# Kernel tuning notes

Hardware: AMD Instinct MI355X
Metric: run time of the kernel (lower is better)

Reference implementation:

```python
import jax, jax.numpy as jnp
import numpy as np

D = 512          # hidden_dim
H_HEADS = 8
DH = D // H_HEADS  # 64
L = 6            # n_layers
P = 8            # patch size
KT = 3           # temporal kernel
Z_DIM = 32
FILM_SCALE = 0.5
ROPE_BASE = 10000.0
EPS = 1e-5


def layer_norm(x, g, b):
    mu = x.mean(-1, keepdims=True)
    var = ((x - mu) ** 2).mean(-1, keepdims=True)
    return (x - mu) * jax.lax.rsqrt(var + EPS) * g + b


def rotate_half(x):
    x1, x2 = jnp.split(x, 2, axis=-1)
    return jnp.concatenate([-x2, x1], axis=-1)


def rope_time(T, dtype):
    half = DH // 2
    inv_freq = ROPE_BASE ** (-(jnp.arange(half, dtype=dtype) / half))  # (half,)
    angles = jnp.arange(T, dtype=dtype)[:, None] * inv_freq[None, :]   # (T, half)
    sin = jnp.concatenate([jnp.sin(angles), jnp.sin(angles)], -1)      # (T, DH)
    cos = jnp.concatenate([jnp.cos(angles), jnp.cos(angles)], -1)
    return sin, cos


def setup_inputs() -> dict:
    key = jax.random.key(0)
    ks = iter(jax.random.split(key, 64))
    n = lambda shape, s=0.02: jax.random.normal(next(ks), shape, jnp.float32) * s
    inp = {
        "x": jax.random.normal(next(ks), (16, 32, 3, 64, 64), jnp.float32),
        "z": jax.random.normal(next(ks), (16, 32, Z_DIM), jnp.float32),
        # tokenizer: CausalConv3d (kt,ph,pw)=(3,8,8), stride (1,8,8)
        "conv_w": n((D, 3, KT, P, P)),
        "conv_b": jnp.zeros((D,), jnp.float32),
        "tok_g": jnp.ones((D,), jnp.float32),
        "tok_b": jnp.zeros((D,), jnp.float32),
        # FiLM from z -> (gamma, beta)
        "film_w": n((Z_DIM, 2 * D)),
        "film_b": jnp.zeros((2 * D,), jnp.float32),
        # transformer blocks (stacked over L)
        "ln1_g": jnp.ones((L, D), jnp.float32), "ln1_b": jnp.zeros((L, D), jnp.float32),
        "kqv_w": n((L, D, 3 * D)), "kqv_b": jnp.zeros((L, 3 * D), jnp.float32),
        "proj_w": n((L, D, D)), "proj_b": jnp.zeros((L, D), jnp.float32),
        "ln2_g": jnp.ones((L, D), jnp.float32), "ln2_b": jnp.zeros((L, D), jnp.float32),
        "mlp_w1": n((L, D, 4 * D)), "mlp_b1": jnp.zeros((L, 4 * D), jnp.float32),
        "mlp_w2": n((L, 4 * D, D)), "mlp_b2": jnp.zeros((L, D), jnp.float32),
        "rs_attn": jnp.full((L,), 0.5, jnp.float32),
        "rs_mlp": jnp.full((L,), 0.5, jnp.float32),
        # scoring head
        "head_g": jnp.ones((D,), jnp.float32), "head_b": jnp.zeros((D,), jnp.float32),
        "head_w": n((D, 1)), "head_bias": jnp.zeros((1,), jnp.float32),
    }
    return inp


def _forward(x, z, conv_w, conv_b, tok_g, tok_b, film_w, film_b,
             ln1_g, ln1_b, kqv_w, kqv_b, proj_w, proj_b, ln2_g, ln2_b,
             mlp_w1, mlp_b1, mlp_w2, mlp_b2, rs_attn, rs_mlp,
             head_g, head_b, head_w, head_bias):
    B, T, C, Himg, Wimg = x.shape
    # ---- SpatialTemporalTokenizer: causal Conv3d (pad time on past only) ----
    xc = jnp.transpose(x, (0, 2, 1, 3, 4))  # [B,C,T,H,W]
    y = jax.lax.conv_general_dilated(
        xc, conv_w, window_strides=(1, P, P),
        padding=[(KT - 1, 0), (0, 0), (0, 0)],
        dimension_numbers=("NCDHW", "OIDHW", "NCDHW"))
    y = y + conv_b[None, :, None, None, None]          # [B,D,T,Hn,Wn]
    Hn, Wn = y.shape[3], y.shape[4]
    tok = jnp.transpose(y, (0, 2, 3, 4, 1)).reshape(B, T, Hn * Wn, D)
    tok = layer_norm(tok, tok_g, tok_b)                 # [B,T,N,D]
    # ---- FiLM conditioning from z ----
    gb = z @ film_w + film_b                            # [B,T,2D]
    gamma, beta = jnp.split(gb, 2, axis=-1)
    tok = (1.0 + FILM_SCALE * gamma)[:, :, None, :] * tok + (FILM_SCALE * beta)[:, :, None, :]
    # ---- spatial pooling -> temporal sequence ----
    h = tok.mean(axis=2)                                # [B,T,D]
    # ---- transformer stack (causal, time RoPE, pre-LN, gated residuals) ----
    sin_t, cos_t = rope_time(T, h.dtype)                # (T, DH)
    causal = jnp.tril(jnp.ones((T, T), bool))
    neg_inf = jnp.finfo(h.dtype).min
    for i in range(L):
        xi = layer_norm(h, ln1_g[i], ln1_b[i])
        kqv = xi @ kqv_w[i] + kqv_b[i]                  # [B,T,3D]
        k, q, v = jnp.split(kqv, 3, axis=-1)            # torch chunk order: k,q,v
        sh = lambda t: t.reshape(B, T, H_HEADS, DH).transpose(0, 2, 1, 3)  # [B,h,T,d]
        q, k, v = sh(q), sh(k), sh(v)
        q = q * cos_t + rotate_half(q) * sin_t
        k = k * cos_t + rotate_half(k) * sin_t
        att = jnp.einsum("bhqd,bhkd->bhqk", q, k) / np.sqrt(DH)
        att = jnp.where(causal[None, None], att, neg_inf)
        att = jax.nn.softmax(att, axis=-1)
        yv = jnp.einsum("bhqk,bhkd->bhqd", att, v)
        yv = yv.transpose(0, 2, 1, 3).reshape(B, T, D)
        attn_out = yv @ proj_w[i] + proj_b[i]
        h = h + rs_attn[i] * attn_out
        x2 = layer_norm(h, ln2_g[i], ln2_b[i])
        m = jax.nn.gelu(x2 @ mlp_w1[i] + mlp_b1[i], approximate=False) @ mlp_w2[i] + mlp_b2[i]
        h = h + rs_mlp[i] * m
    # ---- per-timestep score head ----
    h = layer_norm(h, head_g, head_b)
    score = (h @ head_w + head_bias)[..., 0]            # [B,T]
    return score


def reference(x, z, conv_w, conv_b, tok_g, tok_b, film_w, film_b,
              ln1_g, ln1_b, kqv_w, kqv_b, proj_w, proj_b, ln2_g, ln2_b,
              mlp_w1, mlp_b1, mlp_w2, mlp_b2, rs_attn, rs_mlp,
              head_g, head_b, head_w, head_bias):
    return _forward(x, z, conv_w, conv_b, tok_g, tok_b, film_w, film_b,
                    ln1_g, ln1_b, kqv_w, kqv_b, proj_w, proj_b, ln2_g, ln2_b,
                    mlp_w1, mlp_b1, mlp_w2, mlp_b2, rs_attn, rs_mlp,
                    head_g, head_b, head_w, head_bias)
```

## Files before the change

### kernel.cpp

```cpp
#include <hip/hip_runtime.h>
#include <math.h>

#define EPS 1e-5f

typedef __attribute__((ext_vector_type(8))) short short8;
typedef __attribute__((ext_vector_type(4))) float f32x4;

__device__ __forceinline__ short f2bf(float f) {
    unsigned u = __float_as_uint(f);
    u += 0x7fffu + ((u >> 16) & 1u);
    return (short)(u >> 16);
}
__device__ __forceinline__ float bf2f(short s) {
    return __uint_as_float(((unsigned)(unsigned short)s) << 16);
}
__device__ __forceinline__ void async16(const void* g, void* l) {
    __builtin_amdgcn_global_load_lds(
        (const __attribute__((address_space(1))) unsigned*)g,
        (__attribute__((address_space(3))) unsigned*)l, 16, 0, 0);
}

__device__ __forceinline__ float block_reduce_sum_256(float v, float* red) {
    #pragma unroll
    for (int o = 32; o > 0; o >>= 1) v += __shfl_down(v, o, 64);
    __syncthreads();
    if ((threadIdx.x & 63) == 0) red[threadIdx.x >> 6] = v;
    __syncthreads();
    return red[0] + red[1] + red[2] + red[3];
}

__global__ __launch_bounds__(256) void prep_misc(
    const float* __restrict__ z, const float* __restrict__ fw,
    const float* __restrict__ fb, float* __restrict__ gb,
    const float* __restrict__ conv_w, short* __restrict__ wbf,
    const float* __restrict__ x, short* __restrict__ xbf) {
    __shared__ float zs[32];
    int bi = blockIdx.x, tid = threadIdx.x;
    if (bi < 512) {
        if (tid < 32) zs[tid] = z[bi * 32 + tid];
        __syncthreads();
        for (int j = tid; j < 1024; j += 256) {
            float acc = fb[j];
            #pragma unroll
            for (int k = 0; k < 32; k++) acc = fmaf(zs[k], fw[k * 1024 + j], acc);
            gb[bi * 1024 + j] = acc;
        }
    } else if (bi < 1664) {
        int i = (bi - 512) * 256 + tid;
        wbf[i] = f2bf(conv_w[i]);
    } else {
        int i = (bi - 1664) * 256 + tid;
        float4 a = *(const float4*)(x + (size_t)i * 8);
        float4 b = *(const float4*)(x + (size_t)i * 8 + 4);
        short8 o = {f2bf(a.x), f2bf(a.y), f2bf(a.z), f2bf(a.w),
                    f2bf(b.x), f2bf(b.y), f2bf(b.z), f2bf(b.w)};
        *(short8*)(xbf + (size_t)i * 8) = o;
    }
}

__global__ __launch_bounds__(256) void prep_tcast(
    const float* __restrict__ kqv_w, short* __restrict__ kqvT,
    const float* __restrict__ proj_w, short* __restrict__ projT,
    const float* __restrict__ mlp_w1, short* __restrict__ mlp1T,
    const float* __restrict__ mlp_w2, short* __restrict__ mlp2T) {
    __shared__ float tile[32][33];
    int bi = blockIdx.x;
    const float* src; short* dst; int NT, K, N, rel;
    if (bi < 4608)       { src = kqv_w;  dst = kqvT;  NT = 48; K = 512;  N = 1536; rel = bi; }
    else if (bi < 6144)  { src = proj_w; dst = projT; NT = 16; K = 512;  N = 512;  rel = bi - 4608; }
    else if (bi < 12288) { src = mlp_w1; dst = mlp1T; NT = 64; K = 512;  N = 2048; rel = bi - 6144; }
    else                 { src = mlp_w2; dst = mlp2T; NT = 16; K = 2048; N = 512;  rel = bi - 12288; }
    int per = NT * (K / 32);
    int layer = rel / per, r2 = rel - layer * per;
    int nt = r2 % NT, kt = r2 / NT;
    src += (size_t)layer * K * N;
    dst += (size_t)layer * N * K;
    int n0 = nt * 32, k0 = kt * 32;
    int lx = threadIdx.x & 31, ly = threadIdx.x >> 5;
    #pragma unroll
    for (int i = 0; i < 32; i += 8)
        tile[ly + i][lx] = src[(size_t)(k0 + ly + i) * N + n0 + lx];
    __syncthreads();
    #pragma unroll
    for (int i = 0; i < 32; i += 8)
        dst[(size_t)(n0 + ly + i) * K + k0 + lx] = f2bf(tile[lx][ly + i]);
}

__global__ __launch_bounds__(256) void conv_gemm(
    const short* __restrict__ xbf, const short* __restrict__ wbf,
    const float* __restrict__ cb, short* __restrict__ tok) {
    __shared__ short As[128 * 64];
    __shared__ short Bs[128 * 64];
    int tid = threadIdx.x;
    int n0 = blockIdx.x * 128, m0 = blockIdx.y * 128;
    int wave = tid >> 6, lane = tid & 63, quad = lane >> 4, l16 = lane & 15;
    int wm = wave & 1, wn = wave >> 1;

    int segA[4], tA[4];
    long long base0[4];
    #pragma unroll
    for (int e = 0; e < 4; e++) {
        int p = e * 256 + tid;
        int row = p >> 3;
        segA[e] = (p & 7) ^ (row & 7);
        int m = m0 + row;
        int bt = m >> 6, nn = m & 63;
        int b = bt >> 5, t = bt & 31;
        int hn = nn >> 3, wn2 = nn & 7;
        tA[e] = t;
        base0[e] = (((long long)(b * 32 + t - 2) * 3) << 12)
                   + (long long)(hn * 8) * 64 + wn2 * 8;
    }

    f32x4 acc[4][4];
    #pragma unroll
    for (int mt = 0; mt < 4; mt++)
        #pragma unroll
        for (int nt = 0; nt < 4; nt++) acc[mt][nt] = (f32x4){0.f, 0.f, 0.f, 0.f};

    for (int k0 = 0; k0 < 576; k0 += 64) {
        #pragma unroll
        for (int e = 0; e < 4; e++) {
            int p = e * 256 + tid;
            int n = p >> 3, seg = (p & 7) ^ (n & 7);
            async16(wbf + (size_t)(n0 + n) * 576 + k0 + seg * 8, Bs + p * 8);
        }
        #pragma unroll
        for (int e = 0; e < 4; e++) {
            int p = e * 256 + tid;
            int ks = (k0 >> 3) + segA[e];
            int ch = (ks >= 24) + (ks >= 48);
            int r = ks - ch * 24;
            int kt = r >> 3, ph = r & 7;
            short8 v8 = (short8){0, 0, 0, 0, 0, 0, 0, 0};
            if (tA[e] + kt >= 2)
                v8 = *(const short8*)(xbf + base0[e]
                        + ((long long)(kt * 3 + ch) << 12) + ph * 64);
            *(short8*)(As + p * 8) = v8;
        }
        __syncthreads();
        #pragma unroll
        for (int ksub = 0; ksub < 2; ksub++) {
            int ccb = ksub * 4 + quad;
            short8 af[4], bf[4];
            #pragma unroll
            for (int mt = 0; mt < 4; mt++) {
                int row = wm * 64 + mt * 16 + l16;
                af[mt] = *(const short8*)(As + (row * 8 + (ccb ^ (row & 7))) * 8);
            }
            #pragma unroll
            for (int nt = 0; nt < 4; nt++) {
                int row = wn * 64 + nt * 16 + l16;
                bf[nt] = *(const short8*)(Bs + (row * 8 + (ccb ^ (row & 7))) * 8);
            }
            #pragma unroll
            for (int mt = 0; mt < 4; mt++)
                #pragma unroll
                for (int nt = 0; nt < 4; nt++)
                    acc[mt][nt] = __builtin_amdgcn_mfma_f32_16x16x32_bf16(
                        af[mt], bf[nt], acc[mt][nt], 0, 0, 0);
        }
        __syncthreads();
    }
    #pragma unroll
    for (int mt = 0; mt < 4; mt++)
        #pragma unroll
        for (int nt = 0; nt < 4; nt++)
            #pragma unroll
            for (int reg = 0; reg < 4; reg++) {
                int m = m0 + wm * 64 + mt * 16 + quad * 4 + reg;
                int n = n0 + wn * 64 + nt * 16 + l16;
                tok[(size_t)m * 512 + n] = f2bf(acc[mt][nt][reg] + cb[n]);
            }
}

__global__ __launch_bounds__(256) void tok_post(
    const short* __restrict__ tok, const float* __restrict__ tg,
    const float* __restrict__ tb, const float* __restrict__ gb,
    float* __restrict__ h) {
    __shared__ float mu_s[64], inv_s[64];
    __shared__ float red[4][512];
    int bt = blockIdx.x, tid = threadIdx.x;
    int wave = tid >> 6, lane = tid & 63;
    {
        int tokn = wave * 16 + (lane >> 2), part = lane & 3;
        const short* p = tok + (size_t)(bt * 64 + tokn) * 512 + part * 128;
        float s = 0.f, ss = 0.f;
        #pragma unroll
        for (int i = 0; i < 16; i++) {
            short8 v = *(const short8*)(p + i * 8);
            #pragma unroll
            for (int j = 0; j < 8; j++) {
                float f = bf2f(v[j]);
                s += f; ss += f * f;
            }
        }
        s += __shfl_xor(s, 1, 64); ss += __shfl_xor(ss, 1, 64);
        s += __shfl_xor(s, 2, 64); ss += __shfl_xor(ss, 2, 64);
        if (part == 0) {
            float mu = s * (1.f / 512.f);
            float var = ss * (1.f / 512.f) - mu * mu;
            mu_s[tokn] = mu;
            inv_s[tokn] = rsqrtf(var + EPS);
        }
    }
    __syncthreads();
    float hacc[8] = {0.f, 0.f, 0.f, 0.f, 0.f, 0.f, 0.f, 0.f};
    int c0 = lane * 8;
    for (int it = 0; it < 16; it++) {
        int n = it * 4 + wave;
        float mu = mu_s[n], inv = inv_s[n];
        short8 v = *(const short8*)(tok + (size_t)(bt * 64 + n) * 512 + c0);
        #pragma unroll
        for (int j = 0; j < 8; j++) hacc[j] += (bf2f(v[j]) - mu) * inv;
    }
    #pragma unroll
    for (int j = 0; j < 8; j++) red[wave][c0 + j] = hacc[j];
    __syncthreads();
    #pragma unroll
    for (int cc = 0; cc < 2; cc++) {
        int c = tid + cc * 256;
        float S = red[0][c] + red[1][c] + red[2][c] + red[3][c];
        float G  = 1.f + 0.5f * gb[bt * 1024 + c];
        float Be = 0.5f * gb[bt * 1024 + 512 + c];
        h[bt * 512 + c] = G * (tg[c] * (S * (1.f / 64.f)) + tb[c]) + Be;
    }
}

__global__ __launch_bounds__(256) void attn_fused(
    const float* __restrict__ hsrc, const float* __restrict__ lng,
    const float* __restrict__ lnb, const short* __restrict__ Bw,
    const float* __restrict__ bias, short* __restrict__ yv) {
    __shared__ char smem[57344] __attribute__((aligned(16)));
    __shared__ float mu_s[32], inv_s[32];
    short* As = (short*)smem;
    short* Bs = (short*)(smem + 32768);
    float (*qs)[64] = (float(*)[64])(smem);
    float (*ks)[64] = (float(*)[64])(smem + 8192);
    float (*vs)[64] = (float(*)[64])(smem + 16384);
    float (*qr)[64] = (float(*)[64])(smem + 24576);
    float (*kr)[64] = (float(*)[64])(smem + 32768);
    float (*att)[32] = (float(*)[32])(smem + 40960);
    int blk = blockIdx.x, b = blk >> 3, hh = blk & 7;
    int tid = threadIdx.x;
    int m0 = b * 32;
    {
        int row = tid >> 3, l8 = tid & 7;
        const float* hp = hsrc + (size_t)(m0 + row) * 512 + l8 * 64;
        float s = 0.f, ss = 0.f;
        #pragma unroll
        for (int i = 0; i < 16; i++) {
            float4 v = *(const float4*)(hp + i * 4);
            s += v.x + v.y + v.z + v.w;
            ss += v.x * v.x + v.y * v.y + v.z * v.z + v.w * v.w;
        }
        s += __shfl_xor(s, 1, 64); ss += __shfl_xor(ss, 1, 64);
        s += __shfl_xor(s, 2, 64); ss += __shfl_xor(ss, 2, 64);
        s += __shfl_xor(s, 4, 64); ss += __shfl_xor(ss, 4, 64);
        if (l8 == 0) {
            float mu = s * (1.f / 512.f);
            float var = ss * (1.f / 512.f) - mu * mu;
            mu_s[row] = mu;
            inv_s[row] = rsqrtf(var + EPS);
        }
    }
    __syncthreads();
    #pragma unroll
    for (int e = 0; e < 8; e++) {
        int lc = e * 256 + tid;
        int row = lc >> 6, cc = lc & 63;
        float mu = mu_s[row], inv = inv_s[row];
        const float* hp = hsrc + (size_t)(m0 + row) * 512 + cc * 8;
        float4 a = *(const float4*)hp, b2 = *(const float4*)(hp + 4);
        float4 g0 = *(const float4*)(lng + cc * 8), g1 = *(const float4*)(lng + cc * 8 + 4);
        float4 b0 = *(const float4*)(lnb + cc * 8), b1 = *(const float4*)(lnb + cc * 8 + 4);
        short8 o = {f2bf((a.x - mu) * inv * g0.x + b0.x),
                    f2bf((a.y - mu) * inv * g0.y + b0.y),
                    f2bf((a.z - mu) * inv * g0.z + b0.z),
                    f2bf((a.w - mu) * inv * g0.w + b0.w),
                    f2bf((b2.x - mu) * inv * g1.x + b1.x),
                    f2bf((b2.y - mu) * inv * g1.y + b1.y),
                    f2bf((b2.z - mu) * inv * g1.z + b1.z),
                    f2bf((b2.w - mu) * inv * g1.w + b1.w)};
        *(short8*)(As + (row * 64 + (cc ^ (row & 7))) * 8) = o;
    }
    __syncthreads();
    int wave = tid >> 6, lane = tid & 63, quad = lane >> 4, l16 = lane & 15;
    f32x4 acc[2][3];
    #pragma unroll
    for (int m2 = 0; m2 < 2; m2++)
        #pragma unroll
        for (int g = 0; g < 3; g++) acc[m2][g] = (f32x4){0.f, 0.f, 0.f, 0.f};
    for (int k0 = 0; k0 < 512; k0 += 64) {
        #pragma unroll
        for (int e = 0; e < 6; e++) {
            int p = e * 256 + tid;
            int row = p >> 3, seg = (p & 7) ^ (row & 7);
            int n = ((row >> 6) << 9) + hh * 64 + (row & 63);
            async16(Bw + (size_t)n * 512 + k0 + seg * 8, Bs + p * 8);
        }
        __syncthreads();
        #pragma unroll
        for (int ksub = 0; ksub < 2; ksub++) {
            int ccb = ksub * 4 + quad;
            short8 af[2], bf[3];
            #pragma unroll
            for (int m2 = 0; m2 < 2; m2++) {
                int row = m2 * 16 + l16;
                int cc = (k0 >> 3) + ccb;
                af[m2] = *(const short8*)(As + (row * 64 + (cc ^ (row & 7))) * 8);
            }
            #pragma unroll
            for (int g = 0; g < 3; g++) {
                int row = g * 64 + wave * 16 + l16;
                bf[g] = *(const short8*)(Bs + (row * 8 + (ccb ^ (row & 7))) * 8);
            }
            #pragma unroll
            for (int m2 = 0; m2 < 2; m2++)
                #pragma unroll
                for (int g = 0; g < 3; g++)
                    acc[m2][g] = __builtin_amdgcn_mfma_f32_16x16x32_bf16(
                        af[m2], bf[g], acc[m2][g], 0, 0, 0);
        }
        __syncthreads();
    }
    float bb0 = bias[hh * 64 + wave * 16 + l16];
    float bb1 = bias[512 + hh * 64 + wave * 16 + l16];
    float bb2 = bias[1024 + hh * 64 + wave * 16 + l16];
    int dcol = wave * 16 + l16;
    #pragma unroll
    for (int m2 = 0; m2 < 2; m2++)
        #pragma unroll
        for (int reg = 0; reg < 4; reg++) {
            int tkn = m2 * 16 + quad * 4 + reg;
            ks[tkn][dcol] = acc[m2][0][reg] + bb0;
            qs[tkn][dcol] = acc[m2][1][reg] + bb1;
            vs[tkn][dcol] = acc[m2][2][reg] + bb2;
        }
    __syncthreads();
    const float lnb_c = logf(10000.f) / 32.f;
    for (int idx = tid; idx < 2048; idx += 256) {
        int t = idx >> 6, d = idx & 63;
        int j = d & 31;
        float ang = (float)t * expf(-(float)j * lnb_c);
        float sv = sinf(ang), cv = cosf(ang);
        float qv = qs[t][d], kv = ks[t][d];
        float qo = qs[t][d ^ 32], ko = ks[t][d ^ 32];
        float rq = (d < 32) ? -qo : qo;
        float rk = (d < 32) ? -ko : ko;
        qr[t][d] = qv * cv + rq * sv;
        kr[t][d] = kv * cv + rk * sv;
    }
    __syncthreads();
    #pragma unroll
    for (int l = 0; l < 4; l++) {
        int idx = l * 256 + tid;
        int qt = idx >> 5, kt2 = idx & 31;
        float s;
        if (kt2 > qt) {
            s = -1e30f;
        } else {
            float a = 0.f;
            #pragma unroll
            for (int d = 0; d < 64; d++) a = fmaf(qr[qt][d], kr[kt2][d], a);
            s = a * 0.125f;
        }
        att[qt][kt2] = s;
    }
    __syncthreads();
    if (tid < 32) {
        float m = -1e30f;
        #pragma unroll
        for (int k = 0; k < 32; k++) m = fmaxf(m, att[tid][k]);
        float sum = 0.f;
        #pragma unroll
        for (int k = 0; k < 32; k++) {
            float e = expf(att[tid][k] - m);
            att[tid][k] = e;
            sum += e;
        }
        float inv = 1.f / sum;
        #pragma unroll
        for (int k = 0; k < 32; k++) att[tid][k] *= inv;
    }
    __syncthreads();
    for (int idx = tid; idx < 2048; idx += 256) {
        int t = idx >> 6, d = idx & 63;
        float a = 0.f;
        #pragma unroll
        for (int k = 0; k < 32; k++) a = fmaf(att[t][k], vs[k][d], a);
        yv[(size_t)(b * 32 + t) * 512 + hh * 64 + d] = f2bf(a);
    }
}

__global__ __launch_bounds__(256) void gemm_ln(
    const float* __restrict__ hsrc, const float* __restrict__ lng,
    const float* __restrict__ lnb, const short* __restrict__ Bw,
    const float* __restrict__ bias, int N, int mode,
    float* __restrict__ outf, short* __restrict__ outb) {
    __shared__ short As[32 * 512];
    __shared__ short Bs[128 * 128];
    __shared__ float mu_s[32], inv_s[32];
    int tid = threadIdx.x;
    int m0 = blockIdx.y * 32, n0 = blockIdx.x * 128;
    {
        int row = tid >> 3, l8 = tid & 7;
        const float* hp = hsrc + (size_t)(m0 + row) * 512 + l8 * 64;
        float s = 0.f, ss = 0.f;
        #pragma unroll
        for (int i = 0; i < 16; i++) {
            float4 v = *(const float4*)(hp + i * 4);
            s += v.x + v.y + v.z + v.w;
            ss += v.x * v.x + v.y * v.y + v.z * v.z + v.w * v.w;
        }
        s += __shfl_xor(s, 1, 64); ss += __shfl_xor(ss, 1, 64);
        s += __shfl_xor(s, 2, 64); ss += __shfl_xor(ss, 2, 64);
        s += __shfl_xor(s, 4, 64); ss += __shfl_xor(ss, 4, 64);
        if (l8 == 0) {
            float mu = s * (1.f / 512.f);
            float var = ss * (1.f / 512.f) - mu * mu;
            mu_s[row] = mu;
            inv_s[row] = rsqrtf(var + EPS);
        }
    }
    __syncthreads();
    #pragma unroll
    for (int e = 0; e < 8; e++) {
        int lc = e * 256 + tid;
        int row = lc >> 6, cc = lc & 63;
        float mu = mu_s[row], inv = inv_s[row];
        const float* hp = hsrc + (size_t)(m0 + row) * 512 + cc * 8;
        float4 a = *(const float4*)hp, b = *(const float4*)(hp + 4);
        float4 g0 = *(const float4*)(lng + cc * 8), g1 = *(const float4*)(lng + cc * 8 + 4);
        float4 b0 = *(const float4*)(lnb + cc * 8), b1 = *(const float4*)(lnb + cc * 8 + 4);
        short8 o = {f2bf((a.x - mu) * inv * g0.x + b0.x),
                    f2bf((a.y - mu) * inv * g0.y + b0.y),
                    f2bf((a.z - mu) * inv * g0.z + b0.z),
                    f2bf((a.w - mu) * inv * g0.w + b0.w),
                    f2bf((b.x - mu) * inv * g1.x + b1.x),
                    f2bf((b.y - mu) * inv * g1.y + b1.y),
                    f2bf((b.z - mu) * inv * g1.z + b1.z),
                    f2bf((b.w - mu) * inv * g1.w + b1.w)};
        *(short8*)(As + (row * 64 + (cc ^ (row & 7))) * 8) = o;
    }
    __syncthreads();
    int wave = tid >> 6, lane = tid & 63, quad = lane >> 4, l16 = lane & 15;
    f32x4 acc[2][2];
    #pragma unroll
    for (int a2 = 0; a2 < 2; a2++)
        #pragma unroll
        for (int b2 = 0; b2 < 2; b2++) acc[a2][b2] = (f32x4){0.f, 0.f, 0.f, 0.f};
    for (int k0 = 0; k0 < 512; k0 += 128) {
        #pragma unroll
        for (int e = 0; e < 8; e++) {
            int p = e * 256 + tid;
            int row = p >> 4, seg = (p & 15) ^ (row & 15);
            async16(Bw + (size_t)(n0 + row) * 512 + k0 + seg * 8, Bs + p * 8);
        }
        __syncthreads();
        #pragma unroll
        for (int ksub = 0; ksub < 4; ksub++) {
            int ccb = ksub * 4 + quad;
            short8 af[2], bf[2];
            #pragma unroll
            for (int m2 = 0; m2 < 2; m2++) {
                int row = m2 * 16 + l16;
                int cc = (k0 >> 3) + ccb;
                af[m2] = *(const short8*)(As + (row * 64 + (cc ^ (row & 7))) * 8);
            }
            #pragma unroll
            for (int n2 = 0; n2 < 2; n2++) {
                int row = wave * 32 + n2 * 16 + l16;
                bf[n2] = *(const short8*)(Bs + (row * 16 + (ccb ^ (row & 15))) * 8);
            }
            #pragma unroll
            for (int m2 = 0; m2 < 2; m2++)
                #pragma unroll
                for (int n2 = 0; n2 < 2; n2++)
                    acc[m2][n2] = __builtin_amdgcn_mfma_f32_16x16x32_bf16(
                        af[m2], bf[n2], acc[m2][n2], 0, 0, 0);
        }
        __syncthreads();
    }
    #pragma unroll
    for (int m2 = 0; m2 < 2; m2++)
        #pragma unroll
        for (int n2 = 0; n2 < 2; n2++)
            #pragma unroll
            for (int reg = 0; reg < 4; reg++) {
                int m = m0 + m2 * 16 + quad * 4 + reg;
                int n = n0 + wave * 32 + n2 * 16 + l16;
                float v = acc[m2][n2][reg] + bias[n];
                if (mode == 1) {
                    v = 0.5f * v * (1.f + erff(v * 0.70710678118f));
                    outb[(size_t)m * N + n] = f2bf(v);
                } else {
                    outf[(size_t)m * N + n] = v;
                }
            }
}

__global__ __launch_bounds__(256) void gemm_res(
    const short* __restrict__ Ag, const short* __restrict__ Bw,
    const float* __restrict__ bias, const float* __restrict__ rsPtr,
    float* __restrict__ hm, int K) {
    __shared__ short As[32 * 128];
    __shared__ short Bs[64 * 128];
    int tid = threadIdx.x;
    int m0 = blockIdx.y * 32, n0 = blockIdx.x * 64;
    int wave = tid >> 6, lane = tid & 63, quad = lane >> 4, l16 = lane & 15;
    f32x4 acc[2];
    acc[0] = (f32x4){0.f, 0.f, 0.f, 0.f};
    acc[1] = (f32x4){0.f, 0.f, 0.f, 0.f};
    for (int k0 = 0; k0 < K; k0 += 128) {
        #pragma unroll
        for (int e = 0; e < 2; e++) {
            int p = e * 256 + tid;
            int row = p >> 4, seg = (p & 15) ^ (row & 15);
            async16(Ag + (size_t)(m0 + row) * K + k0 + seg * 8, As + p * 8);
        }
        #pragma unroll
        for (int e = 0; e < 4; e++) {
            int p = e * 256 + tid;
            int row = p >> 4, seg = (p & 15) ^ (row & 15);
            async16(Bw + (size_t)(n0 + row) * K + k0 + seg * 8, Bs + p * 8);
        }
        __syncthreads();
        #pragma unroll
        for (int ksub = 0; ksub < 4; ksub++) {
            int ccb = ksub * 4 + quad;
            short8 bf;
            {
                int row = wave * 16 + l16;
                bf = *(const short8*)(Bs + (row * 16 + (ccb ^ (row & 15))) * 8);
            }
            #pragma unroll
            for (int m2 = 0; m2 < 2; m2++) {
                int row = m2 * 16 + l16;
                short8 af = *(const short8*)(As + (row * 16 + (ccb ^ (row & 15))) * 8);
                acc[m2] = __builtin_amdgcn_mfma_f32_16x16x32_bf16(af, bf, acc[m2], 0, 0, 0);
            }
        }
        __syncthreads();
    }
    float rsv = *rsPtr;
    #pragma unroll
    for (int m2 = 0; m2 < 2; m2++)
        #pragma unroll
        for (int reg = 0; reg < 4; reg++) {
            int m = m0 + m2 * 16 + quad * 4 + reg;
            int n = n0 + wave * 16 + l16;
            size_t off = (size_t)m * 512 + n;
            hm[off] = hm[off] + rsv * (acc[m2][reg] + bias[n]);
        }
}

__global__ __launch_bounds__(256) void head_kernel(
    const float* __restrict__ h, const float* __restrict__ g,
    const float* __restrict__ bb, const float* __restrict__ w,
    const float* __restrict__ bias0, float* __restrict__ out) {
    __shared__ float red[8];
    int token = blockIdx.x, tid = threadIdx.x;
    float v0 = h[token * 512 + tid], v1 = h[token * 512 + tid + 256];
    float s  = block_reduce_sum_256(v0 + v1, red);
    float ss = block_reduce_sum_256(v0 * v0 + v1 * v1, red);
    float mu = s * (1.f / 512.f);
    float var = ss * (1.f / 512.f) - mu * mu;
    float inv = rsqrtf(var + EPS);
    float n0 = (v0 - mu) * inv * g[tid] + bb[tid];
    float n1 = (v1 - mu) * inv * g[tid + 256] + bb[tid + 256];
    float dot = block_reduce_sum_256(n0 * w[tid] + n1 * w[tid + 256], red);
    if (tid == 0) out[token] = dot + bias0[0];
}

extern "C" void kernel_launch(void* const* d_in, const int* in_sizes, int n_in,
                              void* d_out, int out_size, void* d_ws, size_t ws_size,
                              hipStream_t stream) {
    const float* x       = (const float*)d_in[0];
    const float* z       = (const float*)d_in[1];
    const float* conv_w  = (const float*)d_in[2];
    const float* conv_b  = (const float*)d_in[3];
    const float* tok_g   = (const float*)d_in[4];
    const float* tok_b   = (const float*)d_in[5];
    const float* film_w  = (const float*)d_in[6];
    const float* film_b  = (const float*)d_in[7];
    const float* ln1_g   = (const float*)d_in[8];
    const float* ln1_b   = (const float*)d_in[9];
    const float* kqv_w   = (const float*)d_in[10];
    const float* kqv_b   = (const float*)d_in[11];
    const float* proj_w  = (const float*)d_in[12];
    const float* proj_b  = (const float*)d_in[13];
    const float* ln2_g   = (const float*)d_in[14];
    const float* ln2_b   = (const float*)d_in[15];
    const float* mlp_w1  = (const float*)d_in[16];
    const float* mlp_b1  = (const float*)d_in[17];
    const float* mlp_w2  = (const float*)d_in[18];
    const float* mlp_b2  = (const float*)d_in[19];
    const float* rs_attn = (const float*)d_in[20];
    const float* rs_mlp  = (const float*)d_in[21];
    const float* head_g  = (const float*)d_in[22];
    const float* head_b  = (const float*)d_in[23];
    const float* head_w  = (const float*)d_in[24];
    const float* head_bs = (const float*)d_in[25];
    float* out = (float*)d_out;

    float* ws = (float*)d_ws;
    float* gb   = ws;
    float* h    = gb + 524288;
    short* sb = (short*)(h + 262144);
    short* wbf   = sb;
    short* kqvT  = wbf   + 294912;
    short* projT = kqvT  + 4718592;
    short* mlp1T = projT + 1572864;
    short* mlp2T = mlp1T + 6291456;
    short* tokb  = mlp2T + 6291456;
    short* yvb   = tokb  + 16777216;
    short* mbuf  = yvb   + 262144;
    short* xbf   = mbuf  + 1048576;

    prep_misc<<<4736, 256, 0, stream>>>(z, film_w, film_b, gb, conv_w, wbf, x, xbf);
    prep_tcast<<<18432, 256, 0, stream>>>(kqv_w, kqvT, proj_w, projT,
                                          mlp_w1, mlp1T, mlp_w2, mlp2T);

    conv_gemm<<<dim3(4, 256), 256, 0, stream>>>(xbf, wbf, conv_b, tokb);
    tok_post<<<512, 256, 0, stream>>>(tokb, tok_g, tok_b, gb, h);

    for (int i = 0; i < 6; i++) {
        attn_fused<<<128, 256, 0, stream>>>(
            h, ln1_g + i * 512, ln1_b + i * 512,
            kqvT + (size_t)i * 1536 * 512, kqv_b + i * 1536, yvb);
        gemm_res<<<dim3(8, 16), 256, 0, stream>>>(
            yvb, projT + (size_t)i * 512 * 512, proj_b + i * 512,
            rs_attn + i, h, 512);
        gemm_ln<<<dim3(16, 16), 256, 0, stream>>>(
            h, ln2_g + i * 512, ln2_b + i * 512,
            mlp1T + (size_t)i * 2048 * 512, mlp_b1 + i * 2048,
            2048, 1, nullptr, mbuf);
        gemm_res<<<dim3(8, 16), 256, 0, stream>>>(
            mbuf, mlp2T + (size_t)i * 512 * 2048, mlp_b2 + i * 512,
            rs_mlp + i, h, 2048);
    }

    head_kernel<<<512, 256, 0, stream>>>(h, head_g, head_b, head_w, head_bs, out);
}
```

Measured before the change: 549.8 us.

## Fuse conv GEMM with token LayerNorm pooling, split-K residual GEMMs, vectorize transpose

Merges the tokenizer conv GEMM and the tok_post LayerNorm/mean-pool/FiLM pass into one kernel with one block per (b,t). The block computes all 512 output channels for its 64 patches and reduces them in registers, so the large bf16 token buffer is never written or read back. The residual GEMMs (proj and MLP2) now use split-K over blockIdx.z and accumulate into h with atomicAdd, which adds more blocks for small grids at the cost of atomics and non-deterministic summation order. The weight-transpose store also now writes short2 pairs.

```diff
diff --git a/kernel.cpp b/kernel.cpp
--- a/kernel.cpp
+++ b/kernel.cpp
@@ -81,150 +81,144 @@
     for (int i = 0; i < 32; i += 8)
         tile[ly + i][lx] = src[(size_t)(k0 + ly + i) * N + n0 + lx];
     __syncthreads();
-    #pragma unroll
-    for (int i = 0; i < 32; i += 8)
-        dst[(size_t)(n0 + ly + i) * K + k0 + lx] = f2bf(tile[lx][ly + i]);
-}
-
-__global__ __launch_bounds__(256) void conv_gemm(
+    int kp = threadIdx.x & 15, nn = threadIdx.x >> 4;
+    #pragma unroll
+    for (int i = 0; i < 2; i++) {
+        int row = nn + i * 16;
+        short2 o = {f2bf(tile[kp * 2][row]), f2bf(tile[kp * 2 + 1][row])};
+        *(short2*)(dst + (size_t)(n0 + row) * K + k0 + kp * 2) = o;
+    }
+}
+
+__global__ __launch_bounds__(256, 2) void conv_fused(
     const short* __restrict__ xbf, const short* __restrict__ wbf,
-    const float* __restrict__ cb, short* __restrict__ tok) {
-    __shared__ short As[128 * 64];
-    __shared__ short Bs[128 * 64];
+    const float* __restrict__ cb, const float* __restrict__ tg,
+    const float* __restrict__ tb, const float* __restrict__ gb,
+    float* __restrict__ h) {
+    __shared__ short As[64 * 32];
+    __shared__ short Bs[512 * 32];
+    __shared__ float redsum[4][64], redss[4][64];
+    __shared__ float mu_s[64], inv_s[64];
+    int bt = blockIdx.x, b = bt >> 5, t = bt & 31;
     int tid = threadIdx.x;
-    int n0 = blockIdx.x * 128, m0 = blockIdx.y * 128;
     int wave = tid >> 6, lane = tid & 63, quad = lane >> 4, l16 = lane & 15;
-    int wm = wave & 1, wn = wave >> 1;
-
-    int segA[4], tA[4];
-    long long base0[4];
-    #pragma unroll
-    for (int e = 0; e < 4; e++) {
-        int p = e * 256 + tid;
-        int row = p >> 3;
-        segA[e] = (p & 7) ^ (row & 7);
-        int m = m0 + row;
-        int bt = m >> 6, nn = m & 63;
-        int b = bt >> 5, t = bt & 31;
-        int hn = nn >> 3, wn2 = nn & 7;
-        tA[e] = t;
-        base0[e] = (((long long)(b * 32 + t - 2) * 3) << 12)
-                   + (long long)(hn * 8) * 64 + wn2 * 8;
-    }
-
-    f32x4 acc[4][4];
+
+    int rowA = tid >> 2;
+    int cA = (tid & 3) ^ ((rowA >> 1) & 3);
+    int hn = rowA >> 3, wn2 = rowA & 7;
+    long long baseA = (((long long)(b * 32 + t - 2) * 3) << 12)
+                      + (long long)(hn * 8) * 64 + wn2 * 8;
+
+    f32x4 acc[4][8];
     #pragma unroll
     for (int mt = 0; mt < 4; mt++)
         #pragma unroll
-        for (int nt = 0; nt < 4; nt++) acc[mt][nt] = (f32x4){0.f, 0.f, 0.f, 0.f};
-
-    for (int k0 = 0; k0 < 576; k0 += 64) {
-        #pragma unroll
-        for (int e = 0; e < 4; e++) {
-            int p = e * 256 + tid;
-            int n = p >> 3, seg = (p & 7) ^ (n & 7);
-            async16(wbf + (size_t)(n0 + n) * 576 + k0 + seg * 8, Bs + p * 8);
-        }
-        #pragma unroll
-        for (int e = 0; e < 4; e++) {
-            int p = e * 256 + tid;
-            int ks = (k0 >> 3) + segA[e];
+        for (int nt = 0; nt < 8; nt++) acc[mt][nt] = (f32x4){0.f, 0.f, 0.f, 0.f};
+
+    for (int k0 = 0; k0 < 576; k0 += 32) {
+        #pragma unroll
+        for (int e = 0; e < 8; e++) {
+            int s = e * 256 + tid;
+            int n = s >> 2;
+            int c = (s & 3) ^ ((n >> 1) & 3);
+            async16(wbf + (size_t)n * 576 + k0 + c * 8, Bs + s * 8);
+        }
+        {
+            int ks = (k0 >> 3) + cA;
             int ch = (ks >= 24) + (ks >= 48);
             int r = ks - ch * 24;
             int kt = r >> 3, ph = r & 7;
             short8 v8 = (short8){0, 0, 0, 0, 0, 0, 0, 0};
-            if (tA[e] + kt >= 2)
-                v8 = *(const short8*)(xbf + base0[e]
+            if (t + kt >= 2)
+                v8 = *(const short8*)(xbf + baseA
                         + ((long long)(kt * 3 + ch) << 12) + ph * 64);
-            *(short8*)(As + p * 8) = v8;
-        }
-        __syncthreads();
-        #pragma unroll
-        for (int ksub = 0; ksub < 2; ksub++) {
-            int ccb = ksub * 4 + quad;
-            short8 af[4], bf[4];
-            #pragma unroll
-            for (int mt = 0; mt < 4; mt++) {
-                int row = wm * 64 + mt * 16 + l16;
-                af[mt] = *(const short8*)(As + (row * 8 + (ccb ^ (row & 7))) * 8);
-            }
-            #pragma unroll
-            for (int nt = 0; nt < 4; nt++) {
-                int row = wn * 64 + nt * 16 + l16;
-                bf[nt] = *(const short8*)(Bs + (row * 8 + (ccb ^ (row & 7))) * 8);
-            }
-            #pragma unroll
-            for (int mt = 0; mt < 4; mt++)
-                #pragma unroll
-                for (int nt = 0; nt < 4; nt++)
-                    acc[mt][nt] = __builtin_amdgcn_mfma_f32_16x16x32_bf16(
-                        af[mt], bf[nt], acc[mt][nt], 0, 0, 0);
-        }
-        __syncthreads();
+            *(short8*)(As + tid * 8) = v8;
+        }
+        __syncthreads();
+        short8 af[4], bf[8];
+        #pragma unroll
+        for (int mt = 0; mt < 4; mt++) {
+            int row = mt * 16 + l16;
+            int pc = quad ^ ((row >> 1) & 3);
+            af[mt] = *(const short8*)(As + row * 32 + pc * 8);
+        }
+        #pragma unroll
+        for (int nt = 0; nt < 8; nt++) {
+            int row = wave * 128 + nt * 16 + l16;
+            int pc = quad ^ ((row >> 1) & 3);
+            bf[nt] = *(const short8*)(Bs + row * 32 + pc * 8);
+        }
+        #pragma unroll
+        for (int mt = 0; mt < 4; mt++)
+            #pragma unroll
+            for (int nt = 0; nt < 8; nt++)
+                acc[mt][nt] = __builtin_amdgcn_mfma_f32_16x16x32_bf16(
+                    af[mt], bf[nt], acc[mt][nt], 0, 0, 0);
+        __syncthreads();
+    }
+
+    float cbn[8], tgn[8], tbn[8], Gn[8], Ben[8];
+    #pragma unroll
+    for (int nt = 0; nt < 8; nt++) {
+        int n = wave * 128 + nt * 16 + l16;
+        cbn[nt] = cb[n]; tgn[nt] = tg[n]; tbn[nt] = tb[n];
+        Gn[nt]  = 1.f + 0.5f * gb[bt * 1024 + n];
+        Ben[nt] = 0.5f * gb[bt * 1024 + 512 + n];
     }
     #pragma unroll
     for (int mt = 0; mt < 4; mt++)
         #pragma unroll
-        for (int nt = 0; nt < 4; nt++)
-            #pragma unroll
-            for (int reg = 0; reg < 4; reg++) {
-                int m = m0 + wm * 64 + mt * 16 + quad * 4 + reg;
-                int n = n0 + wn * 64 + nt * 16 + l16;
-                tok[(size_t)m * 512 + n] = f2bf(acc[mt][nt][reg] + cb[n]);
-            }
-}
-
-__global__ __launch_bounds__(256) void tok_post(
-    const short* __restrict__ tok, const float* __restrict__ tg,
-    const float* __restrict__ tb, const float* __restrict__ gb,
-    float* __restrict__ h) {
-    __shared__ float mu_s[64], inv_s[64];
-    __shared__ float red[4][512];
-    int bt = blockIdx.x, tid = threadIdx.x;
-    int wave = tid >> 6, lane = tid & 63;
-    {
-        int tokn = wave * 16 + (lane >> 2), part = lane & 3;
-        const short* p = tok + (size_t)(bt * 64 + tokn) * 512 + part * 128;
-        float s = 0.f, ss = 0.f;
-        #pragma unroll
-        for (int i = 0; i < 16; i++) {
-            short8 v = *(const short8*)(p + i * 8);
-            #pragma unroll
-            for (int j = 0; j < 8; j++) {
-                float f = bf2f(v[j]);
-                s += f; ss += f * f;
-            }
-        }
-        s += __shfl_xor(s, 1, 64); ss += __shfl_xor(ss, 1, 64);
-        s += __shfl_xor(s, 2, 64); ss += __shfl_xor(ss, 2, 64);
-        if (part == 0) {
-            float mu = s * (1.f / 512.f);
-            float var = ss * (1.f / 512.f) - mu * mu;
-            mu_s[tokn] = mu;
-            inv_s[tokn] = rsqrtf(var + EPS);
-        }
+        for (int reg = 0; reg < 4; reg++) {
+            float s = 0.f, ss = 0.f;
+            #pragma unroll
+            for (int nt = 0; nt < 8; nt++) {
+                float v = acc[mt][nt][reg] + cbn[nt];
+                s += v; ss += v * v;
+            }
+            #pragma unroll
+            for (int o = 1; o < 16; o <<= 1) {
+                s  += __shfl_xor(s, o, 64);
+                ss += __shfl_xor(ss, o, 64);
+            }
+            if (l16 == 0) {
+                int m = mt * 16 + quad * 4 + reg;
+                redsum[wave][m] = s; redss[wave][m] = ss;
+            }
+        }
+    __syncthreads();
+    if (tid < 64) {
+        float S  = redsum[0][tid] + redsum[1][tid] + redsum[2][tid] + redsum[3][tid];
+        float SS = redss[0][tid] + redss[1][tid] + redss[2][tid] + redss[3][tid];
+        float mu = S * (1.f / 512.f);
+        float var = SS * (1.f / 512.f) - mu * mu;
+        mu_s[tid] = mu; inv_s[tid] = rsqrtf(var + EPS);
     }
     __syncthreads();
     float hacc[8] = {0.f, 0.f, 0.f, 0.f, 0.f, 0.f, 0.f, 0.f};
-    int c0 = lane * 8;
-    for (int it = 0; it < 16; it++) {
-        int n = it * 4 + wave;
-        float mu = mu_s[n], inv = inv_s[n];
-        short8 v = *(const short8*)(tok + (size_t)(bt * 64 + n) * 512 + c0);
-        #pragma unroll
-        for (int j = 0; j < 8; j++) hacc[j] += (bf2f(v[j]) - mu) * inv;
-    }
-    #pragma unroll
-    for (int j = 0; j < 8; j++) red[wave][c0 + j] = hacc[j];
-    __syncthreads();
-    #pragma unroll
-    for (int cc = 0; cc < 2; cc++) {
-        int c = tid + cc * 256;
-        float S = red[0][c] + red[1][c] + red[2][c] + red[3][c];
-        float G  = 1.f + 0.5f * gb[bt * 1024 + c];
-        float Be = 0.5f * gb[bt * 1024 + 512 + c];
-        h[bt * 512 + c] = G * (tg[c] * (S * (1.f / 64.f)) + tb[c]) + Be;
-    }
+    #pragma unroll
+    for (int mt = 0; mt < 4; mt++)
+        #pragma unroll
+        for (int reg = 0; reg < 4; reg++) {
+            int m = mt * 16 + quad * 4 + reg;
+            float mu = mu_s[m], inv = inv_s[m];
+            #pragma unroll
+            for (int nt = 0; nt < 8; nt++) {
+                float v = acc[mt][nt][reg] + cbn[nt];
+                hacc[nt] += (v - mu) * inv;
+            }
+        }
+    #pragma unroll
+    for (int nt = 0; nt < 8; nt++) {
+        hacc[nt] += __shfl_xor(hacc[nt], 16, 64);
+        hacc[nt] += __shfl_xor(hacc[nt], 32, 64);
+    }
+    if (quad == 0)
+        #pragma unroll
+        for (int nt = 0; nt < 8; nt++) {
+            int n = wave * 128 + nt * 16 + l16;
+            h[bt * 512 + n] = Gn[nt] * (tgn[nt] * (hacc[nt] * (1.f / 64.f)) + tbn[nt])
+                              + Ben[nt];
+        }
 }
 
 __global__ __launch_bounds__(256) void attn_fused(
@@ -503,16 +497,17 @@
 __global__ __launch_bounds__(256) void gemm_res(
     const short* __restrict__ Ag, const short* __restrict__ Bw,
     const float* __restrict__ bias, const float* __restrict__ rsPtr,
-    float* __restrict__ hm, int K) {
+    float* __restrict__ hm, int K, int Ks) {
     __shared__ short As[32 * 128];
     __shared__ short Bs[64 * 128];
     int tid = threadIdx.x;
     int m0 = blockIdx.y * 32, n0 = blockIdx.x * 64;
+    int kbase = blockIdx.z * Ks;
     int wave = tid >> 6, lane = tid & 63, quad = lane >> 4, l16 = lane & 15;
     f32x4 acc[2];
     acc[0] = (f32x4){0.f, 0.f, 0.f, 0.f};
     acc[1] = (f32x4){0.f, 0.f, 0.f, 0.f};
-    for (int k0 = 0; k0 < K; k0 += 128) {
+    for (int k0 = kbase; k0 < kbase + Ks; k0 += 128) {
         #pragma unroll
         for (int e = 0; e < 2; e++) {
             int p = e * 256 + tid;
@@ -544,14 +539,15 @@
         __syncthreads();
     }
     float rsv = *rsPtr;
+    bool addb = (blockIdx.z == 0);
     #pragma unroll
     for (int m2 = 0; m2 < 2; m2++)
         #pragma unroll
         for (int reg = 0; reg < 4; reg++) {
             int m = m0 + m2 * 16 + quad * 4 + reg;
             int n = n0 + wave * 16 + l16;
-            size_t off = (size_t)m * 512 + n;
-            hm[off] = hm[off] + rsv * (acc[m2][reg] + bias[n]);
+            float v = acc[m2][reg] + (addb ? bias[n] : 0.f);
+            atomicAdd(&hm[(size_t)m * 512 + n], rsv * v);
         }
 }
 
@@ -613,8 +609,7 @@
     short* projT = kqvT  + 4718592;
     short* mlp1T = projT + 1572864;
     short* mlp2T = mlp1T + 6291456;
-    short* tokb  = mlp2T + 6291456;
-    short* yvb   = tokb  + 16777216;
+    short* yvb   = mlp2T + 6291456;
     short* mbuf  = yvb   + 262144;
     short* xbf   = mbuf  + 1048576;
 
@@ -622,23 +617,22 @@
     prep_tcast<<<18432, 256, 0, stream>>>(kqv_w, kqvT, proj_w, projT,
                                           mlp_w1, mlp1T, mlp_w2, mlp2T);
 
-    conv_gemm<<<dim3(4, 256), 256, 0, stream>>>(xbf, wbf, conv_b, tokb);
-    tok_post<<<512, 256, 0, stream>>>(tokb, tok_g, tok_b, gb, h);
+    conv_fused<<<512, 256, 0, stream>>>(xbf, wbf, conv_b, tok_g, tok_b, gb, h);
 
     for (int i = 0; i < 6; i++) {
         attn_fused<<<128, 256, 0, stream>>>(
             h, ln1_g + i * 512, ln1_b + i * 512,
             kqvT + (size_t)i * 1536 * 512, kqv_b + i * 1536, yvb);
-        gemm_res<<<dim3(8, 16), 256, 0, stream>>>(
+        gemm_res<<<dim3(8, 16, 2), 256, 0, stream>>>(
             yvb, projT + (size_t)i * 512 * 512, proj_b + i * 512,
-            rs_attn + i, h, 512);
+            rs_attn + i, h, 512, 256);
         gemm_ln<<<dim3(16, 16), 256, 0, stream>>>(
             h, ln2_g + i * 512, ln2_b + i * 512,
             mlp1T + (size_t)i * 2048 * 512, mlp_b1 + i * 2048,
             2048, 1, nullptr, mbuf);
-        gemm_res<<<dim3(8, 16), 256, 0, stream>>>(
+        gemm_res<<<dim3(8, 16, 4), 256, 0, stream>>>(
             mbuf, mlp2T + (size_t)i * 512 * 2048, mlp_b2 + i * 512,
-            rs_mlp + i, h, 2048);
+            rs_mlp + i, h, 2048, 512);
     }
 
     head_kernel<<<512, 256, 0, stream>>>(h, head_g, head_b, head_w, head_bs, out);
```

Measured after the change: 511.1 us. 1.08x faster.
